# Kernel tuning notes

Measured on AMD Instinct MI355X. Metric: run time of the kernel, lower is better.

The kernel has to match this reference:

```python
import jax, jax.numpy as jnp
import numpy as np

B, D, H, O, E, K = 8192, 1024, 4096, 1024, 8, 2
HG = H // 2  # gate hidden dim


def setup_inputs() -> dict:
    key = jax.random.key(0)
    ks = jax.random.split(key, 6)
    s1 = 1.0 / np.sqrt(D)
    s2 = 1.0 / np.sqrt(H)
    sg = 1.0 / np.sqrt(HG)
    return {
        "x": jax.random.normal(ks[0], (B, D), jnp.float32),
        "W1": jax.random.normal(ks[1], (E, D, H), jnp.float32) * s1,
        "b1": jnp.zeros((E, H), jnp.float32),
        "W2": jax.random.normal(ks[2], (E, H, O), jnp.float32) * s2,
        "b2": jnp.zeros((E, O), jnp.float32),
        "Wg1": jax.random.normal(ks[3], (D, HG), jnp.float32) * s1,
        "bg1": jnp.zeros((HG,), jnp.float32),
        "Wg2": jax.random.normal(ks[4], (HG, E), jnp.float32) * sg,
        "bg2": jnp.zeros((E,), jnp.float32),
    }


def reference(x, W1, b1, W2, b2, Wg1, bg1, Wg2, bg2):
    # Gate: Linear -> ReLU -> Linear -> softmax over experts
    gate_logits = jax.nn.relu(x @ Wg1 + bg1) @ Wg2 + bg2          # [B, E]
    gate_weights = jax.nn.softmax(gate_logits, axis=1)           # [B, E]

    # Top-k selection and renormalization (second softmax, as in torch)
    top_w, top_idx = jax.lax.top_k(gate_weights, K)              # [B, K]
    top_w = jax.nn.softmax(top_w, axis=1)                        # [B, K]

    # Dense per-expert MLPs (the torch code evaluates every expert)
    h = jax.nn.relu(jnp.einsum('bd,edh->beh', x, W1) + b1)       # [B, E, H]
    expert_outputs = jnp.einsum('beh,eho->beo', h, W2) + b2      # [B, E, O]

    # Gather top-k expert outputs and combine with renormalized weights
    gathered = jnp.take_along_axis(expert_outputs, top_idx[:, :, None], axis=1)  # [B, K, O]
    output = jnp.einsum('bk,bko->bo', top_w, gathered)           # [B, O]

    # Load balancing loss (only expert_fractions feeds the loss; the
    # expert_usage loop in the torch code is dead w.r.t. the returned loss)
    expert_fractions = gate_weights.mean(axis=0)                 # [E]
    cv_loss = jnp.sum((expert_fractions - 1.0 / E) ** 2)

    return output, gate_weights, cv_loss
```

## Files before the change

### kernel.cpp

```cpp
#include <hip/hip_runtime.h>

#define B_  8192
#define D_  1024
#define H_  4096
#define O_  1024
#define E_  8
#define HG_ 2048

typedef _Float16 half8 __attribute__((ext_vector_type(8)));
typedef _Float16 half4 __attribute__((ext_vector_type(4)));
typedef float    f32x4 __attribute__((ext_vector_type(4)));

#define MFMA_F16(a, b, c) __builtin_amdgcn_mfma_f32_16x16x32_f16((a), (b), (c), 0, 0, 0)

typedef const unsigned int __attribute__((address_space(1)))* as1_u32;
typedef unsigned int __attribute__((address_space(3)))* as3_u32;

__device__ __forceinline__ void gload_lds16(const void* g, void* s) {
  __builtin_amdgcn_global_load_lds((as1_u32)(g), (as3_u32)(s), 16, 0, 0);
}

__global__ void zero_small(int* cnt, float* colsum) {
  if (threadIdx.x < E_) { cnt[threadIdx.x] = 0; colsum[threadIdx.x] = 0.f; }
}

__global__ void cvt_x(const float* __restrict__ x, _Float16* __restrict__ xh,
                      _Float16* __restrict__ xl) {
  size_t i = ((size_t)blockIdx.x * 256 + threadIdx.x) * 4;
  float4 v = *(const float4*)(x + i);
  _Float16 h0 = (_Float16)v.x, h1 = (_Float16)v.y, h2 = (_Float16)v.z, h3 = (_Float16)v.w;
  half4 hh = {h0, h1, h2, h3};
  half4 ll = {(_Float16)(v.x - (float)h0), (_Float16)(v.y - (float)h1),
              (_Float16)(v.z - (float)h2), (_Float16)(v.w - (float)h3)};
  *(half4*)(xh + i) = hh;
  *(half4*)(xl + i) = ll;
}

template <bool LO>
__global__ void transpose_cvt(const float* __restrict__ in, _Float16* __restrict__ oh,
                              _Float16* __restrict__ ol, int M, int N) {
  __shared__ float t[32][33];
  const size_t boff = (size_t)blockIdx.z * M * N;
  int bx = blockIdx.x * 32, by = blockIdx.y * 32;
  int tx = threadIdx.x, ty = threadIdx.y;
  const float* src = in + boff;
#pragma unroll
  for (int i = ty; i < 32; i += 8) t[i][tx] = src[(size_t)(by + i) * N + bx + tx];
  __syncthreads();
  _Float16* dh = oh + boff;
#pragma unroll
  for (int i = ty; i < 32; i += 8) {
    float v = t[tx][i];
    size_t oidx = (size_t)(bx + i) * M + by + tx;
    _Float16 h = (_Float16)v;
    dh[oidx] = h;
    if (LO) ol[oidx] = (_Float16)(v - (float)h);
  }
}

__global__ __launch_bounds__(256) void gate_gemm(
    const _Float16* __restrict__ xh, const _Float16* __restrict__ xl,
    const _Float16* __restrict__ wh, const _Float16* __restrict__ wl,
    const float* __restrict__ bg1, float* __restrict__ ghid) {
  __shared__ _Float16 sAh[128 * 32], sAl[128 * 32], sBh[128 * 32], sBl[128 * 32];
  const int tid = threadIdx.x, wave = tid >> 6, lane = tid & 63;
  const int m0 = blockIdx.y * 128, n0 = blockIdx.x * 128;
  const int srow = (wave << 4) + (lane >> 2);
  const int scol = (lane & 3) << 3;
  _Float16* dA0 = sAh + (wave * 16) * 32;
  _Float16* dA1 = sAh + (64 + wave * 16) * 32;
  _Float16* dA0l = sAl + (wave * 16) * 32;
  _Float16* dA1l = sAl + (64 + wave * 16) * 32;
  _Float16* dB0 = sBh + (wave * 16) * 32;
  _Float16* dB1 = sBh + (64 + wave * 16) * 32;
  _Float16* dB0l = sBl + (wave * 16) * 32;
  _Float16* dB1l = sBl + (64 + wave * 16) * 32;
  const _Float16* gA0 = xh + (size_t)(m0 + srow) * D_ + scol;
  const _Float16* gA1 = xh + (size_t)(m0 + 64 + srow) * D_ + scol;
  const _Float16* gA0l = xl + (size_t)(m0 + srow) * D_ + scol;
  const _Float16* gA1l = xl + (size_t)(m0 + 64 + srow) * D_ + scol;
  const _Float16* gB0 = wh + (size_t)(n0 + srow) * D_ + scol;
  const _Float16* gB1 = wh + (size_t)(n0 + 64 + srow) * D_ + scol;
  const _Float16* gB0l = wl + (size_t)(n0 + srow) * D_ + scol;
  const _Float16* gB1l = wl + (size_t)(n0 + 64 + srow) * D_ + scol;
  f32x4 acc[4][4] = {};
  const int wm = wave & 1, wn = wave >> 1, fr = lane & 15, fq = lane >> 4;
  for (int k0 = 0; k0 < D_; k0 += 32) {
    __syncthreads();
    gload_lds16(gA0 + k0, dA0);
    gload_lds16(gA1 + k0, dA1);
    gload_lds16(gA0l + k0, dA0l);
    gload_lds16(gA1l + k0, dA1l);
    gload_lds16(gB0 + k0, dB0);
    gload_lds16(gB1 + k0, dB1);
    gload_lds16(gB0l + k0, dB0l);
    gload_lds16(gB1l + k0, dB1l);
    __syncthreads();
    half8 ah[4], al[4], bh[4], bl[4];
#pragma unroll
    for (int i = 0; i < 4; i++) {
      ah[i] = *(const half8*)(sAh + (wm * 64 + i * 16 + fr) * 32 + fq * 8);
      al[i] = *(const half8*)(sAl + (wm * 64 + i * 16 + fr) * 32 + fq * 8);
      bh[i] = *(const half8*)(sBh + (wn * 64 + i * 16 + fr) * 32 + fq * 8);
      bl[i] = *(const half8*)(sBl + (wn * 64 + i * 16 + fr) * 32 + fq * 8);
    }
#pragma unroll
    for (int mi = 0; mi < 4; mi++)
#pragma unroll
      for (int ni = 0; ni < 4; ni++) {
        acc[mi][ni] = MFMA_F16(ah[mi], bh[ni], acc[mi][ni]);
        acc[mi][ni] = MFMA_F16(ah[mi], bl[ni], acc[mi][ni]);
        acc[mi][ni] = MFMA_F16(al[mi], bh[ni], acc[mi][ni]);
      }
  }
#pragma unroll
  for (int mi = 0; mi < 4; mi++)
#pragma unroll
    for (int i = 0; i < 4; i++) {
      int row = m0 + wm * 64 + mi * 16 + fq * 4 + i;
      float* dst = ghid + (size_t)row * HG_ + n0 + wn * 64;
#pragma unroll
      for (int ni = 0; ni < 4; ni++) {
        int col = ni * 16 + fr;
        dst[col] = fmaxf(acc[mi][ni][i] + bg1[n0 + wn * 64 + col], 0.f);
      }
    }
}

__global__ __launch_bounds__(256) void gate_finish(
    const float* __restrict__ ghid, const float* __restrict__ wg2,
    const float* __restrict__ bg2, float* __restrict__ gw, int* __restrict__ tok,
    float* __restrict__ tkw, int* __restrict__ tkf, int* __restrict__ cnt,
    float* __restrict__ colsum) {
  __shared__ int s_e[32];
  __shared__ float s_p[32];
  __shared__ float s_col[E_];
  __shared__ int s_c[E_], s_c2[E_], s_b[E_];
  const int tid = threadIdx.x, wave = tid >> 6, lane = tid & 63;
  if (tid < E_) { s_col[tid] = 0.f; s_c[tid] = 0; s_c2[tid] = 0; }
  __syncthreads();
  for (int it = 0; it < 4; it++) {
    int b = blockIdx.x * 16 + wave * 4 + it;
    const float* g = ghid + (size_t)b * HG_;
    float l[8] = {0, 0, 0, 0, 0, 0, 0, 0};
    for (int j = lane; j < HG_; j += 64) {
      float gv = g[j];
      float4 w0 = *(const float4*)(wg2 + (size_t)j * 8);
      float4 w1 = *(const float4*)(wg2 + (size_t)j * 8 + 4);
      l[0] += gv * w0.x; l[1] += gv * w0.y; l[2] += gv * w0.z; l[3] += gv * w0.w;
      l[4] += gv * w1.x; l[5] += gv * w1.y; l[6] += gv * w1.z; l[7] += gv * w1.w;
    }
#pragma unroll
    for (int off = 32; off; off >>= 1)
#pragma unroll
      for (int r = 0; r < 8; r++) l[r] += __shfl_xor(l[r], off);
    if (lane == 0) {
      float w[8];
      float mx = -1e30f;
#pragma unroll
      for (int r = 0; r < 8; r++) { l[r] += bg2[r]; mx = fmaxf(mx, l[r]); }
      float s = 0.f;
#pragma unroll
      for (int r = 0; r < 8; r++) { w[r] = expf(l[r] - mx); s += w[r]; }
      float inv = 1.f / s;
#pragma unroll
      for (int r = 0; r < 8; r++) w[r] *= inv;
      for (int r = 0; r < 8; r++) {
        gw[(size_t)b * 8 + r] = w[r];
        atomicAdd(&s_col[r], w[r]);
      }
      int i1 = 0;
      for (int r = 1; r < 8; r++) if (w[r] > w[i1]) i1 = r;
      int i2 = (i1 == 0) ? 1 : 0;
      for (int r = 0; r < 8; r++) if (r != i1 && w[r] > w[i2]) i2 = r;
      float e2 = expf(w[i2] - w[i1]);
      float p1 = 1.f / (1.f + e2), p2 = e2 / (1.f + e2);
      int sl = (wave * 4 + it) * 2;
      s_e[sl] = i1; s_p[sl] = p1;
      s_e[sl + 1] = i2; s_p[sl + 1] = p2;
    }
  }
  __syncthreads();
  if (tid < 32) atomicAdd(&s_c[s_e[tid]], 1);
  __syncthreads();
  if (tid < E_) s_b[tid] = atomicAdd(&cnt[tid], s_c[tid]);
  __syncthreads();
  if (tid < 32) {
    int e = s_e[tid];
    int slot = s_b[e] + atomicAdd(&s_c2[e], 1);
    int bb = blockIdx.x * 16 + (tid >> 1);
    tok[e * B_ + slot] = bb;
    tkw[e * B_ + slot] = s_p[tid];
    tkf[e * B_ + slot] = tid & 1;
  }
  if (tid < E_) atomicAdd(&colsum[tid], s_col[tid]);
}

__global__ void prefix_cv(const int* __restrict__ cnt, int* __restrict__ basep,
                          const float* __restrict__ colsum, float* __restrict__ cvout) {
  if (threadIdx.x == 0) {
    int s = 0;
    for (int e = 0; e < E_; e++) { basep[e] = s; s += cnt[e]; }
    float cv = 0.f;
    for (int e = 0; e < E_; e++) {
      float f = colsum[e] * (1.f / B_) - 1.f / E_;
      cv += f * f;
    }
    *cvout = cv;
  }
}

__global__ __launch_bounds__(256) void expert_gemm1(
    const _Float16* __restrict__ xh, const _Float16* __restrict__ w1t,
    const float* __restrict__ b1, const int* __restrict__ tok,
    const int* __restrict__ cnt, const int* __restrict__ basep,
    _Float16* __restrict__ hbuf) {
  const int e = blockIdx.y >> 6, mt = blockIdx.y & 63;
  const int ce = cnt[e];
  if (mt * 128 >= ce) return;
  __shared__ _Float16 sA[128 * 32], sB[128 * 32];
  const int tid = threadIdx.x, wave = tid >> 6, lane = tid & 63;
  const int n0 = blockIdx.x * 128;
  const int srow = (wave << 4) + (lane >> 2), scol = (lane & 3) << 3;
  int r0 = mt * 128 + srow, r1 = r0 + 64;
  if (r0 > ce - 1) r0 = ce - 1;
  if (r1 > ce - 1) r1 = ce - 1;
  const int t0 = tok[e * B_ + r0], t1 = tok[e * B_ + r1];
  const _Float16* gA0 = xh + (size_t)t0 * D_ + scol;
  const _Float16* gA1 = xh + (size_t)t1 * D_ + scol;
  const _Float16* wte = w1t + (size_t)e * H_ * D_;
  const _Float16* gB0 = wte + (size_t)(n0 + srow) * D_ + scol;
  const _Float16* gB1 = wte + (size_t)(n0 + 64 + srow) * D_ + scol;
  _Float16* dA0 = sA + (wave * 16) * 32;
  _Float16* dA1 = sA + (64 + wave * 16) * 32;
  _Float16* dB0 = sB + (wave * 16) * 32;
  _Float16* dB1 = sB + (64 + wave * 16) * 32;
  f32x4 acc[4][4] = {};
  const int wm = wave & 1, wn = wave >> 1, fr = lane & 15, fq = lane >> 4;
  for (int k0 = 0; k0 < D_; k0 += 32) {
    __syncthreads();
    gload_lds16(gA0 + k0, dA0);
    gload_lds16(gA1 + k0, dA1);
    gload_lds16(gB0 + k0, dB0);
    gload_lds16(gB1 + k0, dB1);
    __syncthreads();
    half8 a[4], b[4];
#pragma unroll
    for (int i = 0; i < 4; i++) {
      a[i] = *(const half8*)(sA + (wm * 64 + i * 16 + fr) * 32 + fq * 8);
      b[i] = *(const half8*)(sB + (wn * 64 + i * 16 + fr) * 32 + fq * 8);
    }
#pragma unroll
    for (int mi = 0; mi < 4; mi++)
#pragma unroll
      for (int ni = 0; ni < 4; ni++) acc[mi][ni] = MFMA_F16(a[mi], b[ni], acc[mi][ni]);
  }
  const int base = basep[e];
  float bv[4];
#pragma unroll
  for (int ni = 0; ni < 4; ni++) bv[ni] = b1[e * H_ + n0 + wn * 64 + ni * 16 + fr];
#pragma unroll
  for (int mi = 0; mi < 4; mi++)
#pragma unroll
    for (int i = 0; i < 4; i++) {
      int rloc = mt * 128 + wm * 64 + mi * 16 + fq * 4 + i;
      if (rloc < ce) {
        _Float16* dst = hbuf + (size_t)(base + rloc) * H_ + n0 + wn * 64;
#pragma unroll
        for (int ni = 0; ni < 4; ni++)
          dst[ni * 16 + fr] = (_Float16)fmaxf(acc[mi][ni][i] + bv[ni], 0.f);
      }
    }
}

__global__ __launch_bounds__(256) void expert_gemm2(
    const _Float16* __restrict__ hbuf, const _Float16* __restrict__ w2t,
    const float* __restrict__ b2, const int* __restrict__ tok,
    const float* __restrict__ tkw, const int* __restrict__ tkf,
    const int* __restrict__ cnt, const int* __restrict__ basep,
    float* __restrict__ obuf) {
  const int e = blockIdx.y >> 6, mt = blockIdx.y & 63;
  const int ce = cnt[e];
  if (mt * 128 >= ce) return;
  __shared__ _Float16 sA[128 * 32], sB[128 * 32];
  const int tid = threadIdx.x, wave = tid >> 6, lane = tid & 63;
  const int n0 = blockIdx.x * 128;
  const int srow = (wave << 4) + (lane >> 2), scol = (lane & 3) << 3;
  const int base = basep[e];
  int r0 = mt * 128 + srow, r1 = r0 + 64;
  if (r0 > ce - 1) r0 = ce - 1;
  if (r1 > ce - 1) r1 = ce - 1;
  const _Float16* gA0 = hbuf + (size_t)(base + r0) * H_ + scol;
  const _Float16* gA1 = hbuf + (size_t)(base + r1) * H_ + scol;
  const _Float16* wte = w2t + (size_t)e * O_ * H_;
  const _Float16* gB0 = wte + (size_t)(n0 + srow) * H_ + scol;
  const _Float16* gB1 = wte + (size_t)(n0 + 64 + srow) * H_ + scol;
  _Float16* dA0 = sA + (wave * 16) * 32;
  _Float16* dA1 = sA + (64 + wave * 16) * 32;
  _Float16* dB0 = sB + (wave * 16) * 32;
  _Float16* dB1 = sB + (64 + wave * 16) * 32;
  f32x4 acc[4][4] = {};
  const int wm = wave & 1, wn = wave >> 1, fr = lane & 15, fq = lane >> 4;
  for (int k0 = 0; k0 < H_; k0 += 32) {
    __syncthreads();
    gload_lds16(gA0 + k0, dA0);
    gload_lds16(gA1 + k0, dA1);
    gload_lds16(gB0 + k0, dB0);
    gload_lds16(gB1 + k0, dB1);
    __syncthreads();
    half8 a[4], b[4];
#pragma unroll
    for (int i = 0; i < 4; i++) {
      a[i] = *(const half8*)(sA + (wm * 64 + i * 16 + fr) * 32 + fq * 8);
      b[i] = *(const half8*)(sB + (wn * 64 + i * 16 + fr) * 32 + fq * 8);
    }
#pragma unroll
    for (int mi = 0; mi < 4; mi++)
#pragma unroll
      for (int ni = 0; ni < 4; ni++) acc[mi][ni] = MFMA_F16(a[mi], b[ni], acc[mi][ni]);
  }
  float bv[4];
#pragma unroll
  for (int ni = 0; ni < 4; ni++) bv[ni] = b2[e * O_ + n0 + wn * 64 + ni * 16 + fr];
#pragma unroll
  for (int mi = 0; mi < 4; mi++)
#pragma unroll
    for (int i = 0; i < 4; i++) {
      int rloc = mt * 128 + wm * 64 + mi * 16 + fq * 4 + i;
      if (rloc < ce) {
        int t = tok[e * B_ + rloc];
        float p = tkw[e * B_ + rloc];
        int f = tkf[e * B_ + rloc];
        float* dst = obuf + ((size_t)t * 2 + f) * O_ + n0 + wn * 64;
#pragma unroll
        for (int ni = 0; ni < 4; ni++)
          dst[ni * 16 + fr] = p * (acc[mi][ni][i] + bv[ni]);
      }
    }
}

__global__ void combine(const float* __restrict__ obuf, float* __restrict__ out) {
  size_t i = (size_t)blockIdx.x * 256 + threadIdx.x;
  const float4* o4 = (const float4*)obuf;
  size_t b = i >> 8, c = i & 255;
  float4 u = o4[(b * 2) * 256 + c];
  float4 v = o4[(b * 2 + 1) * 256 + c];
  float4 w = {u.x + v.x, u.y + v.y, u.z + v.z, u.w + v.w};
  ((float4*)out)[i] = w;
}

extern "C" void kernel_launch(void* const* d_in, const int* in_sizes, int n_in,
                              void* d_out, int out_size, void* d_ws, size_t ws_size,
                              hipStream_t stream) {
  const float* x = (const float*)d_in[0];
  const float* W1 = (const float*)d_in[1];
  const float* b1 = (const float*)d_in[2];
  const float* W2 = (const float*)d_in[3];
  const float* b2 = (const float*)d_in[4];
  const float* Wg1 = (const float*)d_in[5];
  const float* bg1 = (const float*)d_in[6];
  const float* Wg2 = (const float*)d_in[7];
  const float* bg2 = (const float*)d_in[8];

  float* out = (float*)d_out;
  float* gw = out + (size_t)B_ * O_;
  float* cv = gw + (size_t)B_ * E_;

  char* w = (char*)d_ws;
  const size_t OFF_XH = 0;
  const size_t OFF_XL = OFF_XH + (size_t)B_ * D_ * 2;
  const size_t OFF_WG1H = OFF_XL + (size_t)B_ * D_ * 2;
  const size_t OFF_WG1L = OFF_WG1H + (size_t)HG_ * D_ * 2;
  const size_t OFF_WT = OFF_WG1L + (size_t)HG_ * D_ * 2;
  const size_t OFF_GHID = OFF_WT + (size_t)E_ * H_ * D_ * 2;
  const size_t OFF_HBUF = OFF_GHID + (size_t)B_ * HG_ * 4;
  const size_t OFF_TOK = OFF_HBUF + (size_t)B_ * 2 * H_ * 2;
  const size_t OFF_TKW = OFF_TOK + (size_t)E_ * B_ * 4;
  const size_t OFF_TKF = OFF_TKW + (size_t)E_ * B_ * 4;
  const size_t OFF_CNT = OFF_TKF + (size_t)E_ * B_ * 4;
  const size_t OFF_COL = OFF_CNT + 64;
  const size_t OFF_BASE = OFF_COL + 64;
  const size_t WS_NEED = OFF_BASE + 64;
  if (ws_size < WS_NEED) return;

  _Float16* xh = (_Float16*)(w + OFF_XH);
  _Float16* xl = (_Float16*)(w + OFF_XL);
  _Float16* wg1h = (_Float16*)(w + OFF_WG1H);
  _Float16* wg1l = (_Float16*)(w + OFF_WG1L);
  _Float16* wt = (_Float16*)(w + OFF_WT);
  float* ghid = (float*)(w + OFF_GHID);
  float* obuf = (float*)(w + OFF_GHID);
  _Float16* hbuf = (_Float16*)(w + OFF_HBUF);
  int* tok = (int*)(w + OFF_TOK);
  float* tkw = (float*)(w + OFF_TKW);
  int* tkf = (int*)(w + OFF_TKF);
  int* cnt = (int*)(w + OFF_CNT);
  float* colsum = (float*)(w + OFF_COL);
  int* basep = (int*)(w + OFF_BASE);

  zero_small<<<1, 64, 0, stream>>>(cnt, colsum);
  cvt_x<<<(B_ * D_) / (256 * 4), 256, 0, stream>>>(x, xh, xl);
  transpose_cvt<true><<<dim3(HG_ / 32, D_ / 32, 1), dim3(32, 8), 0, stream>>>(
      Wg1, wg1h, wg1l, D_, HG_);
  transpose_cvt<false><<<dim3(H_ / 32, D_ / 32, E_), dim3(32, 8), 0, stream>>>(
      W1, wt, nullptr, D_, H_);
  gate_gemm<<<dim3(HG_ / 128, B_ / 128), 256, 0, stream>>>(xh, xl, wg1h, wg1l, bg1, ghid);
  gate_finish<<<B_ / 16, 256, 0, stream>>>(ghid, Wg2, bg2, gw, tok, tkw, tkf, cnt, colsum);
  prefix_cv<<<1, 64, 0, stream>>>(cnt, basep, colsum, cv);
  expert_gemm1<<<dim3(H_ / 128, E_ * 64), 256, 0, stream>>>(xh, wt, b1, tok, cnt, basep, hbuf);
  transpose_cvt<false><<<dim3(O_ / 32, H_ / 32, E_), dim3(32, 8), 0, stream>>>(
      W2, wt, nullptr, H_, O_);
  expert_gemm2<<<dim3(O_ / 128, E_ * 64), 256, 0, stream>>>(hbuf, wt, b2, tok, tkw, tkf,
                                                            cnt, basep, obuf);
  combine<<<(B_ * O_) / (256 * 4), 256, 0, stream>>>(obuf, out);
}
```

Measured before the change: 985.6 us.

## Compact expert tile scheduling, deepen K tiles, and reorganize LDS layouts for conflict-free loads

Builds a compact list of (expert, m-tile) pairs in prefix_cv so the expert GEMMs launch only about as many row tiles as needed instead of E*64 mostly-empty blocks. The expert GEMMs double the K step to 64, halving barrier and loop overhead per tile. The gate and expert GEMMs switch to a fragment-major LDS layout meant to avoid bank conflicts on the MFMA operand reads. The transpose/convert kernel now writes half4 vectors instead of scalar stores. The fixed grid bound of 135 tiles could in principle be one short of the worst case.

```diff
diff --git a/kernel.cpp b/kernel.cpp
--- a/kernel.cpp
+++ b/kernel.cpp
@@ -6,6 +6,7 @@
 #define O_  1024
 #define E_  8
 #define HG_ 2048
+#define MAXT_ 135
 
 typedef _Float16 half8 __attribute__((ext_vector_type(8)));
 typedef _Float16 half4 __attribute__((ext_vector_type(4)));
@@ -19,6 +20,7 @@
 __device__ __forceinline__ void gload_lds16(const void* g, void* s) {
   __builtin_amdgcn_global_load_lds((as1_u32)(g), (as3_u32)(s), 16, 0, 0);
 }
+
 
 __global__ void zero_small(int* cnt, float* colsum) {
   if (threadIdx.x < E_) { cnt[threadIdx.x] = 0; colsum[threadIdx.x] = 0.f; }
@@ -47,62 +49,61 @@
 #pragma unroll
   for (int i = ty; i < 32; i += 8) t[i][tx] = src[(size_t)(by + i) * N + bx + tx];
   __syncthreads();
-  _Float16* dh = oh + boff;
-#pragma unroll
-  for (int i = ty; i < 32; i += 8) {
-    float v = t[tx][i];
-    size_t oidx = (size_t)(bx + i) * M + by + tx;
-    _Float16 h = (_Float16)v;
-    dh[oidx] = h;
-    if (LO) ol[oidx] = (_Float16)(v - (float)h);
+  int tid = ty * 32 + tx;
+  int rr = tid >> 3, cq = tid & 7;
+  float v0 = t[cq * 4 + 0][rr], v1 = t[cq * 4 + 1][rr];
+  float v2 = t[cq * 4 + 2][rr], v3 = t[cq * 4 + 3][rr];
+  half4 h = {(_Float16)v0, (_Float16)v1, (_Float16)v2, (_Float16)v3};
+  size_t o = boff + (size_t)(bx + rr) * M + by + cq * 4;
+  *(half4*)(oh + o) = h;
+  if (LO) {
+    half4 l = {(_Float16)(v0 - (float)h[0]), (_Float16)(v1 - (float)h[1]),
+               (_Float16)(v2 - (float)h[2]), (_Float16)(v3 - (float)h[3])};
+    *(half4*)(ol + o) = l;
   }
 }
 
 __global__ __launch_bounds__(256) void gate_gemm(
-    const _Float16* __restrict__ xh, const _Float16* __restrict__ xl,
-    const _Float16* __restrict__ wh, const _Float16* __restrict__ wl,
+    const _Float16* __restrict__ xh, const _Float16* __restrict__ wh,
     const float* __restrict__ bg1, float* __restrict__ ghid) {
   __shared__ _Float16 sAh[128 * 32], sAl[128 * 32], sBh[128 * 32], sBl[128 * 32];
-  const int tid = threadIdx.x, wave = tid >> 6, lane = tid & 63;
+  const int tid = threadIdx.x, wave = tid >> 6;
+  const int lane = tid & 63, fr = lane & 15, fq = lane >> 4;
   const int m0 = blockIdx.y * 128, n0 = blockIdx.x * 128;
-  const int srow = (wave << 4) + (lane >> 2);
-  const int scol = (lane & 3) << 3;
-  _Float16* dA0 = sAh + (wave * 16) * 32;
-  _Float16* dA1 = sAh + (64 + wave * 16) * 32;
-  _Float16* dA0l = sAl + (wave * 16) * 32;
-  _Float16* dA1l = sAl + (64 + wave * 16) * 32;
-  _Float16* dB0 = sBh + (wave * 16) * 32;
-  _Float16* dB1 = sBh + (64 + wave * 16) * 32;
-  _Float16* dB0l = sBl + (wave * 16) * 32;
-  _Float16* dB1l = sBl + (64 + wave * 16) * 32;
-  const _Float16* gA0 = xh + (size_t)(m0 + srow) * D_ + scol;
-  const _Float16* gA1 = xh + (size_t)(m0 + 64 + srow) * D_ + scol;
-  const _Float16* gA0l = xl + (size_t)(m0 + srow) * D_ + scol;
-  const _Float16* gA1l = xl + (size_t)(m0 + 64 + srow) * D_ + scol;
-  const _Float16* gB0 = wh + (size_t)(n0 + srow) * D_ + scol;
-  const _Float16* gB1 = wh + (size_t)(n0 + 64 + srow) * D_ + scol;
-  const _Float16* gB0l = wl + (size_t)(n0 + srow) * D_ + scol;
-  const _Float16* gB1l = wl + (size_t)(n0 + 64 + srow) * D_ + scol;
+  const int wm = wave & 1, wn = wave >> 1;
+  const size_t XL = (size_t)B_ * D_;
+  const size_t WL = (size_t)HG_ * D_;
+
+  const _Float16* srcA[2];
+  const _Float16* srcB[2];
+#pragma unroll
+  for (int j = 0; j < 2; j++) {
+    int c = j * 256 + tid;
+    int g = c >> 6, kg = (c >> 4) & 3, r = c & 15;
+    srcA[j] = xh + (size_t)(m0 + g * 16 + r) * D_ + kg * 8;
+    srcB[j] = wh + (size_t)(n0 + g * 16 + r) * D_ + kg * 8;
+  }
   f32x4 acc[4][4] = {};
-  const int wm = wave & 1, wn = wave >> 1, fr = lane & 15, fq = lane >> 4;
   for (int k0 = 0; k0 < D_; k0 += 32) {
     __syncthreads();
-    gload_lds16(gA0 + k0, dA0);
-    gload_lds16(gA1 + k0, dA1);
-    gload_lds16(gA0l + k0, dA0l);
-    gload_lds16(gA1l + k0, dA1l);
-    gload_lds16(gB0 + k0, dB0);
-    gload_lds16(gB1 + k0, dB1);
-    gload_lds16(gB0l + k0, dB0l);
-    gload_lds16(gB1l + k0, dB1l);
+#pragma unroll
+    for (int j = 0; j < 2; j++) {
+      int lb = (j * 256 + wave * 64) * 8;
+      gload_lds16(srcA[j] + k0, sAh + lb);
+      gload_lds16(srcA[j] + XL + k0, sAl + lb);
+      gload_lds16(srcB[j] + k0, sBh + lb);
+      gload_lds16(srcB[j] + WL + k0, sBl + lb);
+    }
     __syncthreads();
     half8 ah[4], al[4], bh[4], bl[4];
 #pragma unroll
     for (int i = 0; i < 4; i++) {
-      ah[i] = *(const half8*)(sAh + (wm * 64 + i * 16 + fr) * 32 + fq * 8);
-      al[i] = *(const half8*)(sAl + (wm * 64 + i * 16 + fr) * 32 + fq * 8);
-      bh[i] = *(const half8*)(sBh + (wn * 64 + i * 16 + fr) * 32 + fq * 8);
-      bl[i] = *(const half8*)(sBl + (wn * 64 + i * 16 + fr) * 32 + fq * 8);
+      int ca = ((wm * 4 + i) * 64 + fq * 16 + fr) * 8;
+      int cb = ((wn * 4 + i) * 64 + fq * 16 + fr) * 8;
+      ah[i] = *(const half8*)(sAh + ca);
+      al[i] = *(const half8*)(sAl + ca);
+      bh[i] = *(const half8*)(sBh + cb);
+      bl[i] = *(const half8*)(sBl + cb);
     }
 #pragma unroll
     for (int mi = 0; mi < 4; mi++)
@@ -197,10 +198,17 @@
 }
 
 __global__ void prefix_cv(const int* __restrict__ cnt, int* __restrict__ basep,
-                          const float* __restrict__ colsum, float* __restrict__ cvout) {
+                          const float* __restrict__ colsum, float* __restrict__ cvout,
+                          int* __restrict__ tile_e, int* __restrict__ tile_mt,
+                          int* __restrict__ ntiles) {
   if (threadIdx.x == 0) {
-    int s = 0;
-    for (int e = 0; e < E_; e++) { basep[e] = s; s += cnt[e]; }
+    int s = 0, nt = 0;
+    for (int e = 0; e < E_; e++) {
+      basep[e] = s;
+      for (int t = 0; t * 128 < cnt[e]; t++) { tile_e[nt] = e; tile_mt[nt] = t; nt++; }
+      s += cnt[e];
+    }
+    ntiles[0] = nt;
     float cv = 0.f;
     for (int e = 0; e < E_; e++) {
       float f = colsum[e] * (1.f / B_) - 1.f / E_;
@@ -214,46 +222,53 @@
     const _Float16* __restrict__ xh, const _Float16* __restrict__ w1t,
     const float* __restrict__ b1, const int* __restrict__ tok,
     const int* __restrict__ cnt, const int* __restrict__ basep,
-    _Float16* __restrict__ hbuf) {
-  const int e = blockIdx.y >> 6, mt = blockIdx.y & 63;
+    const int* __restrict__ tile_e, const int* __restrict__ tile_mt,
+    const int* __restrict__ ntiles, _Float16* __restrict__ hbuf) {
+  const int idx = blockIdx.y;
+  if (idx >= ntiles[0]) return;
+  const int e = tile_e[idx], mt = tile_mt[idx];
   const int ce = cnt[e];
-  if (mt * 128 >= ce) return;
-  __shared__ _Float16 sA[128 * 32], sB[128 * 32];
-  const int tid = threadIdx.x, wave = tid >> 6, lane = tid & 63;
+  __shared__ _Float16 sA[128 * 64], sB[128 * 64];
+  const int tid = threadIdx.x, wave = tid >> 6;
+  const int lane = tid & 63, fr = lane & 15, fq = lane >> 4;
   const int n0 = blockIdx.x * 128;
-  const int srow = (wave << 4) + (lane >> 2), scol = (lane & 3) << 3;
-  int r0 = mt * 128 + srow, r1 = r0 + 64;
-  if (r0 > ce - 1) r0 = ce - 1;
-  if (r1 > ce - 1) r1 = ce - 1;
-  const int t0 = tok[e * B_ + r0], t1 = tok[e * B_ + r1];
-  const _Float16* gA0 = xh + (size_t)t0 * D_ + scol;
-  const _Float16* gA1 = xh + (size_t)t1 * D_ + scol;
+  const int wm = wave & 1, wn = wave >> 1;
   const _Float16* wte = w1t + (size_t)e * H_ * D_;
-  const _Float16* gB0 = wte + (size_t)(n0 + srow) * D_ + scol;
-  const _Float16* gB1 = wte + (size_t)(n0 + 64 + srow) * D_ + scol;
-  _Float16* dA0 = sA + (wave * 16) * 32;
-  _Float16* dA1 = sA + (64 + wave * 16) * 32;
-  _Float16* dB0 = sB + (wave * 16) * 32;
-  _Float16* dB1 = sB + (64 + wave * 16) * 32;
+  const _Float16* srcA[4];
+  const _Float16* srcB[4];
+#pragma unroll
+  for (int j = 0; j < 4; j++) {
+    int c = j * 256 + tid;
+    int g = c >> 7, kg = (c >> 4) & 7, r = c & 15;
+    int rowA = mt * 128 + g * 16 + r;
+    if (rowA > ce - 1) rowA = ce - 1;
+    int t = tok[e * B_ + rowA];
+    srcA[j] = xh + (size_t)t * D_ + kg * 8;
+    srcB[j] = wte + (size_t)(n0 + g * 16 + r) * D_ + kg * 8;
+  }
   f32x4 acc[4][4] = {};
-  const int wm = wave & 1, wn = wave >> 1, fr = lane & 15, fq = lane >> 4;
-  for (int k0 = 0; k0 < D_; k0 += 32) {
-    __syncthreads();
-    gload_lds16(gA0 + k0, dA0);
-    gload_lds16(gA1 + k0, dA1);
-    gload_lds16(gB0 + k0, dB0);
-    gload_lds16(gB1 + k0, dB1);
-    __syncthreads();
-    half8 a[4], b[4];
-#pragma unroll
-    for (int i = 0; i < 4; i++) {
-      a[i] = *(const half8*)(sA + (wm * 64 + i * 16 + fr) * 32 + fq * 8);
-      b[i] = *(const half8*)(sB + (wn * 64 + i * 16 + fr) * 32 + fq * 8);
-    }
-#pragma unroll
-    for (int mi = 0; mi < 4; mi++)
-#pragma unroll
-      for (int ni = 0; ni < 4; ni++) acc[mi][ni] = MFMA_F16(a[mi], b[ni], acc[mi][ni]);
+  for (int k0 = 0; k0 < D_; k0 += 64) {
+    __syncthreads();
+#pragma unroll
+    for (int j = 0; j < 4; j++) {
+      int lb = (j * 256 + wave * 64) * 8;
+      gload_lds16(srcA[j] + k0, sA + lb);
+      gload_lds16(srcB[j] + k0, sB + lb);
+    }
+    __syncthreads();
+#pragma unroll
+    for (int kk = 0; kk < 2; kk++) {
+      half8 a[4], b[4];
+#pragma unroll
+      for (int i = 0; i < 4; i++) {
+        a[i] = *(const half8*)(sA + ((wm * 4 + i) * 128 + (kk * 4 + fq) * 16 + fr) * 8);
+        b[i] = *(const half8*)(sB + ((wn * 4 + i) * 128 + (kk * 4 + fq) * 16 + fr) * 8);
+      }
+#pragma unroll
+      for (int mi = 0; mi < 4; mi++)
+#pragma unroll
+        for (int ni = 0; ni < 4; ni++) acc[mi][ni] = MFMA_F16(a[mi], b[ni], acc[mi][ni]);
+    }
   }
   const int base = basep[e];
   float bv[4];
@@ -278,46 +293,53 @@
     const float* __restrict__ b2, const int* __restrict__ tok,
     const float* __restrict__ tkw, const int* __restrict__ tkf,
     const int* __restrict__ cnt, const int* __restrict__ basep,
-    float* __restrict__ obuf) {
-  const int e = blockIdx.y >> 6, mt = blockIdx.y & 63;
+    const int* __restrict__ tile_e, const int* __restrict__ tile_mt,
+    const int* __restrict__ ntiles, float* __restrict__ obuf) {
+  const int idx = blockIdx.y;
+  if (idx >= ntiles[0]) return;
+  const int e = tile_e[idx], mt = tile_mt[idx];
   const int ce = cnt[e];
-  if (mt * 128 >= ce) return;
-  __shared__ _Float16 sA[128 * 32], sB[128 * 32];
-  const int tid = threadIdx.x, wave = tid >> 6, lane = tid & 63;
+  const int base = basep[e];
+  __shared__ _Float16 sA[128 * 64], sB[128 * 64];
+  const int tid = threadIdx.x, wave = tid >> 6;
+  const int lane = tid & 63, fr = lane & 15, fq = lane >> 4;
   const int n0 = blockIdx.x * 128;
-  const int srow = (wave << 4) + (lane >> 2), scol = (lane & 3) << 3;
-  const int base = basep[e];
-  int r0 = mt * 128 + srow, r1 = r0 + 64;
-  if (r0 > ce - 1) r0 = ce - 1;
-  if (r1 > ce - 1) r1 = ce - 1;
-  const _Float16* gA0 = hbuf + (size_t)(base + r0) * H_ + scol;
-  const _Float16* gA1 = hbuf + (size_t)(base + r1) * H_ + scol;
+  const int wm = wave & 1, wn = wave >> 1;
   const _Float16* wte = w2t + (size_t)e * O_ * H_;
-  const _Float16* gB0 = wte + (size_t)(n0 + srow) * H_ + scol;
-  const _Float16* gB1 = wte + (size_t)(n0 + 64 + srow) * H_ + scol;
-  _Float16* dA0 = sA + (wave * 16) * 32;
-  _Float16* dA1 = sA + (64 + wave * 16) * 32;
-  _Float16* dB0 = sB + (wave * 16) * 32;
-  _Float16* dB1 = sB + (64 + wave * 16) * 32;
+  const _Float16* srcA[4];
+  const _Float16* srcB[4];
+#pragma unroll
+  for (int j = 0; j < 4; j++) {
+    int c = j * 256 + tid;
+    int g = c >> 7, kg = (c >> 4) & 7, r = c & 15;
+    int rowA = mt * 128 + g * 16 + r;
+    if (rowA > ce - 1) rowA = ce - 1;
+    srcA[j] = hbuf + (size_t)(base + rowA) * H_ + kg * 8;
+    srcB[j] = wte + (size_t)(n0 + g * 16 + r) * H_ + kg * 8;
+  }
   f32x4 acc[4][4] = {};
-  const int wm = wave & 1, wn = wave >> 1, fr = lane & 15, fq = lane >> 4;
-  for (int k0 = 0; k0 < H_; k0 += 32) {
-    __syncthreads();
-    gload_lds16(gA0 + k0, dA0);
-    gload_lds16(gA1 + k0, dA1);
-    gload_lds16(gB0 + k0, dB0);
-    gload_lds16(gB1 + k0, dB1);
-    __syncthreads();
-    half8 a[4], b[4];
-#pragma unroll
-    for (int i = 0; i < 4; i++) {
-      a[i] = *(const half8*)(sA + (wm * 64 + i * 16 + fr) * 32 + fq * 8);
-      b[i] = *(const half8*)(sB + (wn * 64 + i * 16 + fr) * 32 + fq * 8);
-    }
-#pragma unroll
-    for (int mi = 0; mi < 4; mi++)
-#pragma unroll
-      for (int ni = 0; ni < 4; ni++) acc[mi][ni] = MFMA_F16(a[mi], b[ni], acc[mi][ni]);
+  for (int k0 = 0; k0 < H_; k0 += 64) {
+    __syncthreads();
+#pragma unroll
+    for (int j = 0; j < 4; j++) {
+      int lb = (j * 256 + wave * 64) * 8;
+      gload_lds16(srcA[j] + k0, sA + lb);
+      gload_lds16(srcB[j] + k0, sB + lb);
+    }
+    __syncthreads();
+#pragma unroll
+    for (int kk = 0; kk < 2; kk++) {
+      half8 a[4], b[4];
+#pragma unroll
+      for (int i = 0; i < 4; i++) {
+        a[i] = *(const half8*)(sA + ((wm * 4 + i) * 128 + (kk * 4 + fq) * 16 + fr) * 8);
+        b[i] = *(const half8*)(sB + ((wn * 4 + i) * 128 + (kk * 4 + fq) * 16 + fr) * 8);
+      }
+#pragma unroll
+      for (int mi = 0; mi < 4; mi++)
+#pragma unroll
+        for (int ni = 0; ni < 4; ni++) acc[mi][ni] = MFMA_F16(a[mi], b[ni], acc[mi][ni]);
+    }
   }
   float bv[4];
 #pragma unroll
@@ -380,7 +402,10 @@
   const size_t OFF_CNT = OFF_TKF + (size_t)E_ * B_ * 4;
   const size_t OFF_COL = OFF_CNT + 64;
   const size_t OFF_BASE = OFF_COL + 64;
-  const size_t WS_NEED = OFF_BASE + 64;
+  const size_t OFF_TE = OFF_BASE + 64;
+  const size_t OFF_TM = OFF_TE + 640;
+  const size_t OFF_NT = OFF_TM + 640;
+  const size_t WS_NEED = OFF_NT + 64;
   if (ws_size < WS_NEED) return;
 
   _Float16* xh = (_Float16*)(w + OFF_XH);
@@ -397,6 +422,9 @@
   int* cnt = (int*)(w + OFF_CNT);
   float* colsum = (float*)(w + OFF_COL);
   int* basep = (int*)(w + OFF_BASE);
+  int* tile_e = (int*)(w + OFF_TE);
+  int* tile_mt = (int*)(w + OFF_TM);
+  int* ntiles = (int*)(w + OFF_NT);
 
   zero_small<<<1, 64, 0, stream>>>(cnt, colsum);
   cvt_x<<<(B_ * D_) / (256 * 4), 256, 0, stream>>>(x, xh, xl);
@@ -404,13 +432,15 @@
       Wg1, wg1h, wg1l, D_, HG_);
   transpose_cvt<false><<<dim3(H_ / 32, D_ / 32, E_), dim3(32, 8), 0, stream>>>(
       W1, wt, nullptr, D_, H_);
-  gate_gemm<<<dim3(HG_ / 128, B_ / 128), 256, 0, stream>>>(xh, xl, wg1h, wg1l, bg1, ghid);
+  gate_gemm<<<dim3(HG_ / 128, B_ / 128), 256, 0, stream>>>(xh, wg1h, bg1, ghid);
   gate_finish<<<B_ / 16, 256, 0, stream>>>(ghid, Wg2, bg2, gw, tok, tkw, tkf, cnt, colsum);
-  prefix_cv<<<1, 64, 0, stream>>>(cnt, basep, colsum, cv);
-  expert_gemm1<<<dim3(H_ / 128, E_ * 64), 256, 0, stream>>>(xh, wt, b1, tok, cnt, basep, hbuf);
+  prefix_cv<<<1, 64, 0, stream>>>(cnt, basep, colsum, cv, tile_e, tile_mt, ntiles);
+  expert_gemm1<<<dim3(H_ / 128, MAXT_), 256, 0, stream>>>(xh, wt, b1, tok, cnt, basep,
+                                                          tile_e, tile_mt, ntiles, hbuf);
   transpose_cvt<false><<<dim3(O_ / 32, H_ / 32, E_), dim3(32, 8), 0, stream>>>(
       W2, wt, nullptr, H_, O_);
-  expert_gemm2<<<dim3(O_ / 128, E_ * 64), 256, 0, stream>>>(hbuf, wt, b2, tok, tkw, tkf,
-                                                            cnt, basep, obuf);
+  expert_gemm2<<<dim3(O_ / 128, MAXT_), 256, 0, stream>>>(hbuf, wt, b2, tok, tkw, tkf,
+                                                          cnt, basep, tile_e, tile_mt,
+                                                          ntiles, obuf);
   combine<<<(B_ * O_) / (256 * 4), 256, 0, stream>>>(obuf, out);
 }
```

After: 1.234 ms. 25.2% more time.
